# Optimization experiments

Hardware: AMD Instinct MI355X
Metric: run time of the kernel (lower is better)

The kernel has to match this reference:

```python
import jax, jax.numpy as jnp
import numpy as np

D = 4096      # per-region feature dim (input_feature_dims)
OBJ = 20      # regions per frame (memory row = 20*4096)
M = 1000      # temporal_mem_size
K = 1         # temporal_K


def l2norm(x, axis=-1, eps=1e-12):
    # torch F.normalize: x / clamp_min(||x||, eps)
    n = jnp.linalg.norm(x, axis=axis, keepdims=True)
    return x / jnp.maximum(n, eps)


def setup_inputs() -> dict:
    key = jax.random.key(0)
    k1, k2, k3, k4, k5 = jax.random.split(key, 5)
    B, Q, F_ = 4, 4, 20
    return {
        "QR_frm_weight_p": jax.random.normal(k1, (B, Q, F_), jnp.float32),
        "input_pos_feature": jax.random.normal(k2, (B, F_, OBJ, D), jnp.float32),
        "mem1": jax.random.normal(k3, (M, OBJ * D), jnp.float32),
        "mem2": jax.random.normal(k4, (M, OBJ * D), jnp.float32),
        "rand_idx": jax.random.randint(k5, (B, Q, K), 0, F_ - K),
    }


def reference(QR_frm_weight_p, input_pos_feature, mem1, mem2, rand_idx):
    B, Q, F_ = QR_frm_weight_p.shape

    # top-K high-attention frames and a random low-attention frame per query
    _, high_idx = jax.lax.top_k(QR_frm_weight_p, K)              # [B,Q,K]
    _, low_all = jax.lax.top_k(-QR_frm_weight_p, F_ - K)         # smallest, asc
    low_idx = jnp.take_along_axis(low_all, rand_idx, axis=-1)    # [B,Q,K]

    # CVPR feature branch: L2-normalize region features
    R = l2norm(input_pos_feature)                                # [B,F,OBJ,D]

    # max-pool over regions, L2-normalize, then nearest memory slot
    R_max = l2norm(jnp.max(R, axis=2).reshape(-1, D))            # [B*F, D]
    mem1_mp = l2norm(jnp.max(mem1.reshape(M, OBJ, D), axis=1))   # [M, D]
    mem2_mp = l2norm(jnp.max(mem2.reshape(M, OBJ, D), axis=1))   # [M, D]
    sim1 = jnp.argmax(R_max @ mem1_mp.T, axis=-1)                # [B*F]
    Rp_updated = mem1[sim1].reshape(B, F_, OBJ, D)
    sim2 = jnp.argmax(R_max @ mem2_mp.T, axis=-1)
    Rn_updated = mem2[sim2].reshape(B, F_, OBJ, D)

    b_ix = jnp.arange(B)[:, None, None]                          # [B,1,1]
    q_ix = jnp.arange(Q)[None, :, None]                          # [1,Q,1]

    # gather selected frames: [B,Q,K,OBJ,D] -> [Q,B,K,OBJ,D]
    R_high = jnp.transpose(R[b_ix, high_idx], (1, 0, 2, 3, 4))
    R_low = jnp.transpose(R[b_ix, low_idx], (1, 0, 2, 3, 4))

    # Rn: copy of R per query, high-attention frames replaced by mem2
    # counterfactuals gathered at LOW indices (as in the torch code, where
    # `splits` still holds the low-region splits at that point).
    Rn = jnp.broadcast_to(R[:, None], (B, Q, F_, OBJ, D))
    Rn = Rn.at[b_ix, q_ix, high_idx].set(Rn_updated[b_ix, low_idx])
    Rn = jnp.transpose(Rn, (1, 0, 2, 3, 4))                      # [Q,B,F,OBJ,D]

    # Rp: low-attention frames replaced by mem1 entries at low indices
    Rp = jnp.broadcast_to(R[:, None], (B, Q, F_, OBJ, D))
    Rp = Rp.at[b_ix, q_ix, low_idx].set(Rp_updated[b_ix, low_idx])
    Rp = jnp.transpose(Rp, (1, 0, 2, 3, 4))                      # [Q,B,F,OBJ,D]

    # nearest-memory assignment for selected high/low frames
    R_high_mp = l2norm(jnp.max(R_high.reshape(-1, OBJ, D), axis=1))
    R_low_mp = l2norm(jnp.max(R_low.reshape(-1, OBJ, D), axis=1))
    high_sim = jnp.argmax(R_high_mp @ mem2_mp.T, axis=-1)        # [Q*B*K]
    low_sim = jnp.argmax(R_low_mp @ mem1_mp.T, axis=-1)

    return Rp, Rn, high_sim, low_sim
```

## Files before the change

### kernel.cpp

```cpp
#include <hip/hip_runtime.h>

#define D 4096
#define OBJ 20
#define M_MEM 1000
#define F_ 20
#define FRAME_F4 20480
#define RP_F4 6553600
#define OUT_TAIL 52428800

typedef float vf4 __attribute__((ext_vector_type(4)));

__device__ __forceinline__ float4 f4max(float4 a, float4 b){
  return make_float4(fmaxf(a.x,b.x), fmaxf(a.y,b.y), fmaxf(a.z,b.z), fmaxf(a.w,b.w));
}
__device__ __forceinline__ float4 f4scale(float4 a, float s){
  return make_float4(a.x*s, a.y*s, a.z*s, a.w*s);
}
__device__ __forceinline__ double f4ss(float4 a){
  return (double)a.x*a.x + (double)a.y*a.y + (double)a.z*a.z + (double)a.w*a.w;
}
__device__ __forceinline__ void ntst(float4* p, float4 v){
  vf4 t; t.x = v.x; t.y = v.y; t.z = v.z; t.w = v.w;
  __builtin_nontemporal_store(t, (vf4*)p);
}
__device__ __forceinline__ float4 ntld(const float4* p){
  vf4 t = __builtin_nontemporal_load((const vf4*)p);
  return make_float4(t.x, t.y, t.z, t.w);
}

__device__ __forceinline__ unsigned int fkey(float f){
  unsigned int b = __float_as_uint(f);
  return (b & 0x80000000u) ? ~b : (b | 0x80000000u);
}

__device__ __forceinline__ double blockReduce256(double v){
  #pragma unroll
  for (int off = 32; off > 0; off >>= 1) v += __shfl_down(v, off, 64);
  __shared__ double sh[4];
  int w = threadIdx.x >> 6;
  if ((threadIdx.x & 63) == 0) sh[w] = v;
  __syncthreads();
  return sh[0] + sh[1] + sh[2] + sh[3];
}

__global__ void k_fused1(const float* __restrict__ x,
                         const float* __restrict__ mem1, const float* __restrict__ mem2,
                         const float* __restrict__ qr, const int* __restrict__ rand_idx,
                         float* __restrict__ mpn1, float* __restrict__ mpn2,
                         float* __restrict__ rmaxn, float* __restrict__ inv_norm,
                         unsigned long long* __restrict__ packed,
                         int* __restrict__ high_idx, int* __restrict__ low_idx){
  int blk = blockIdx.x;
  int tid = threadIdx.x;
  if (blk >= 80 && blk < 2080){
    int id = blk - 80;
    const float* mem; float* outp; int m;
    if (id < M_MEM){ mem = mem1; outp = mpn1; m = id; }
    else           { mem = mem2; outp = mpn2; m = id - M_MEM; }
    const float4* base = (const float4*)mem + (size_t)m * FRAME_F4;
    float4 mv[4];
    #pragma unroll
    for (int i = 0; i < 4; i++) mv[i] = make_float4(-INFINITY,-INFINITY,-INFINITY,-INFINITY);
    for (int o = 0; o < OBJ; o++){
      const float4* p = base + o*1024;
      #pragma unroll
      for (int i = 0; i < 4; i++) mv[i] = f4max(mv[i], ntld(p + tid + i*256));
    }
    double ss = 0.0;
    #pragma unroll
    for (int i = 0; i < 4; i++) ss += f4ss(mv[i]);
    ss = blockReduce256(ss);
    float rinv = (float)(1.0 / fmax(sqrt(ss), 1e-12));
    float4* o4 = (float4*)outp + (size_t)m * 1024;
    #pragma unroll
    for (int i = 0; i < 4; i++) o4[tid + i*256] = f4scale(mv[i], rinv);
  } else if (blk < 80){
    __shared__ float sinv[OBJ];
    int w = tid >> 6, lane = tid & 63;
    const float4* base = (const float4*)x + (size_t)blk * FRAME_F4;
    for (int o = w*5; o < w*5 + 5; o++){
      const float4* p = base + o*1024;
      double ss = 0.0;
      #pragma unroll
      for (int j = 0; j < 16; j++) ss += f4ss(__ldg(p + j*64 + lane));
      #pragma unroll
      for (int off = 32; off > 0; off >>= 1) ss += __shfl_down(ss, off, 64);
      if (lane == 0){
        float inv = (float)(1.0 / fmax(sqrt(ss), 1e-12));
        sinv[o] = inv;
        inv_norm[blk*OBJ + o] = inv;
      }
    }
    __syncthreads();
    float4 mv[4];
    #pragma unroll
    for (int i = 0; i < 4; i++) mv[i] = make_float4(-INFINITY,-INFINITY,-INFINITY,-INFINITY);
    for (int o = 0; o < OBJ; o++){
      float s = sinv[o];
      const float4* p = base + o*1024;
      #pragma unroll
      for (int i = 0; i < 4; i++) mv[i] = f4max(mv[i], f4scale(__ldg(p + tid + i*256), s));
    }
    double ss = 0.0;
    #pragma unroll
    for (int i = 0; i < 4; i++) ss += f4ss(mv[i]);
    ss = blockReduce256(ss);
    float rinv = (float)(1.0 / fmax(sqrt(ss), 1e-12));
    float4* outp = (float4*)rmaxn + (size_t)blk * 1024;
    #pragma unroll
    for (int i = 0; i < 4; i++) outp[tid + i*256] = f4scale(mv[i], rinv);
  } else {
    int t = tid;
    if (t < 160) packed[t] = 0ull;
    if (t < 16){
      float wv[F_];
      for (int f = 0; f < F_; f++) wv[f] = qr[t*F_ + f];
      int hi = 0; float hv = wv[0];
      for (int f = 1; f < F_; f++) if (wv[f] > hv){ hv = wv[f]; hi = f; }
      int r = rand_idx[t];
      bool used[F_];
      for (int f = 0; f < F_; f++) used[f] = false;
      used[hi] = true;
      int li = 0;
      for (int it = 0; it <= r; it++){
        int bi = -1; float bv = INFINITY;
        for (int f = 0; f < F_; f++) if (!used[f] && wv[f] < bv){ bv = wv[f]; bi = f; }
        used[bi] = true; li = bi;
      }
      high_idx[t] = hi; low_idx[t] = li;
    }
  }
}

__global__ void __launch_bounds__(256, 2)
k_dots(const float* __restrict__ mpn1, const float* __restrict__ mpn2,
       const float* __restrict__ rmaxn,
       unsigned long long* __restrict__ packed){
  int blk = blockIdx.x;
  int which = blk / 250;
  int chunk = blk % 250;
  const float* mpn = which ? mpn2 : mpn1;
  __shared__ float4 rows[4*1024];
  const float4* src = (const float4*)mpn + (size_t)chunk * 4096;
  for (int i = threadIdx.x; i < 4096; i += 256) rows[i] = ntld(src + i);
  __syncthreads();
  int w = threadIdx.x >> 6, lane = threadIdx.x & 63;
  const float4* rbase = (const float4*)rmaxn + (size_t)(w*20) * 1024 + lane;
  float acc[20][4];
  #pragma unroll
  for (int j = 0; j < 20; j++){
    acc[j][0] = 0.f; acc[j][1] = 0.f; acc[j][2] = 0.f; acc[j][3] = 0.f;
  }
  for (int i = 0; i < 16; i++){
    float4 m0 = rows[       i*64 + lane];
    float4 m1 = rows[1024 + i*64 + lane];
    float4 m2 = rows[2048 + i*64 + lane];
    float4 m3 = rows[3072 + i*64 + lane];
    #pragma unroll
    for (int j = 0; j < 20; j++){
      float4 r = __ldg(rbase + (size_t)j*1024 + i*64);
      acc[j][0] += r.x*m0.x + r.y*m0.y + r.z*m0.z + r.w*m0.w;
      acc[j][1] += r.x*m1.x + r.y*m1.y + r.z*m1.z + r.w*m1.w;
      acc[j][2] += r.x*m2.x + r.y*m2.y + r.z*m2.z + r.w*m2.w;
      acc[j][3] += r.x*m3.x + r.y*m3.y + r.z*m3.z + r.w*m3.w;
    }
  }
  unsigned long long* slot = packed + which*80 + w*20;
  #pragma unroll
  for (int j = 0; j < 20; j++){
    float s0 = acc[j][0], s1 = acc[j][1], s2 = acc[j][2], s3 = acc[j][3];
    #pragma unroll
    for (int off = 32; off > 0; off >>= 1){
      s0 += __shfl_down(s0, off, 64);
      s1 += __shfl_down(s1, off, 64);
      s2 += __shfl_down(s2, off, 64);
      s3 += __shfl_down(s3, off, 64);
    }
    if (lane == 0){
      float best = s0; int bi = 0;
      if (s1 > best){ best = s1; bi = 1; }
      if (s2 > best){ best = s2; bi = 2; }
      if (s3 > best){ best = s3; bi = 3; }
      unsigned long long pk = ((unsigned long long)fkey(best) << 32) |
                              (unsigned int)(chunk*4 + bi);
      atomicMax(slot + j, pk);
    }
  }
}

__global__ void k_write(const float* __restrict__ x, const float* __restrict__ inv_norm,
                        const float* __restrict__ mem1, const float* __restrict__ mem2,
                        const int* __restrict__ high_idx, const int* __restrict__ low_idx,
                        const unsigned long long* __restrict__ packed,
                        float* __restrict__ outp){
  int bid = blockIdx.x;
  int tid = threadIdx.x;
  int fid = bid >> 3;
  int part = bid & 7;
  int q = fid / 80;
  int rem = fid - q*80;
  int b = rem / F_;
  int f = rem - b*F_;
  int t16 = b*4 + q;
  int lo = __ldg(low_idx + t16), hi = __ldg(high_idx + t16);

  if (bid == 0 && tid < 16){
    int tb = tid >> 2, tq = tid & 3;
    int thi = __ldg(high_idx + tid), tlo = __ldg(low_idx + tid);
    int s2hi = (int)(unsigned int)__ldg(packed + 80 + tb*F_ + thi);
    int s1lo = (int)(unsigned int)__ldg(packed +      tb*F_ + tlo);
    outp[OUT_TAIL      + tq*4 + tb] = (float)s2hi;
    outp[OUT_TAIL + 16 + tq*4 + tb] = (float)s1lo;
  }

  __shared__ float sinv[OBJ];
  if (tid < OBJ) sinv[tid] = inv_norm[(b*F_ + f)*OBJ + tid];
  __syncthreads();

  const float4* xf = (const float4*)x + (size_t)(b*F_ + f)*FRAME_F4;
  float4* o4 = (float4*)outp;
  size_t fbase = (size_t)fid * FRAME_F4;

  if (f == lo){
    int rpRow = (int)(unsigned int)__ldg(packed + b*F_ + lo);
    const float4* m1p = (const float4*)mem1 + (size_t)rpRow * FRAME_F4;
    #pragma unroll
    for (int k = 0; k < 10; k++){
      int e4 = part*2560 + k*256 + tid;
      float s = sinv[(part*10 + k) >> 2];
      float4 xn = f4scale(__ldg(xf + e4), s);
      ntst(o4 + fbase + e4, __ldg(m1p + e4));
      ntst(o4 + RP_F4 + fbase + e4, xn);
    }
  } else if (f == hi){
    int rnRow = (int)(unsigned int)__ldg(packed + 80 + b*F_ + lo);
    const float4* m2p = (const float4*)mem2 + (size_t)rnRow * FRAME_F4;
    #pragma unroll
    for (int k = 0; k < 10; k++){
      int e4 = part*2560 + k*256 + tid;
      float s = sinv[(part*10 + k) >> 2];
      float4 xn = f4scale(__ldg(xf + e4), s);
      ntst(o4 + fbase + e4, xn);
      ntst(o4 + RP_F4 + fbase + e4, __ldg(m2p + e4));
    }
  } else {
    #pragma unroll
    for (int k = 0; k < 10; k++){
      int e4 = part*2560 + k*256 + tid;
      float s = sinv[(part*10 + k) >> 2];
      float4 xn = f4scale(__ldg(xf + e4), s);
      ntst(o4 + fbase + e4, xn);
      ntst(o4 + RP_F4 + fbase + e4, xn);
    }
  }
}

extern "C" void kernel_launch(void* const* d_in, const int* in_sizes, int n_in,
                              void* d_out, int out_size, void* d_ws, size_t ws_size,
                              hipStream_t stream) {
  const float* qr       = (const float*)d_in[0];
  const float* x        = (const float*)d_in[1];
  const float* mem1     = (const float*)d_in[2];
  const float* mem2     = (const float*)d_in[3];
  const int*   rand_idx = (const int*)  d_in[4];
  float* outp = (float*)d_out;

  float* mpn1     = (float*)d_ws;
  float* mpn2     = mpn1 + 4096000;
  float* rmaxn    = mpn2 + 4096000;
  float* inv_norm = rmaxn + 327680;
  unsigned long long* packed = (unsigned long long*)(inv_norm + 1600);
  int*   high_idx = (int*)(packed + 160);
  int*   low_idx  = high_idx + 16;

  k_fused1<<<2081, 256, 0, stream>>>(x, mem1, mem2, qr, rand_idx,
                                     mpn1, mpn2, rmaxn, inv_norm,
                                     packed, high_idx, low_idx);
  k_dots  <<<500,  256, 0, stream>>>(mpn1, mpn2, rmaxn, packed);
  k_write <<<2560, 256, 0, stream>>>(x, inv_norm, mem1, mem2,
                                     high_idx, low_idx, packed, outp);
}
```

Before: 792.1 us.

## Reuse normalized frame across all queries in write kernel; drop LDS staging in dots

```diff
diff --git a/kernel.cpp b/kernel.cpp
--- a/kernel.cpp
+++ b/kernel.cpp
@@ -132,18 +132,14 @@
   }
 }
 
-__global__ void __launch_bounds__(256, 2)
+__global__ void __launch_bounds__(256, 3)
 k_dots(const float* __restrict__ mpn1, const float* __restrict__ mpn2,
        const float* __restrict__ rmaxn,
        unsigned long long* __restrict__ packed){
   int blk = blockIdx.x;
   int which = blk / 250;
   int chunk = blk % 250;
-  const float* mpn = which ? mpn2 : mpn1;
-  __shared__ float4 rows[4*1024];
-  const float4* src = (const float4*)mpn + (size_t)chunk * 4096;
-  for (int i = threadIdx.x; i < 4096; i += 256) rows[i] = ntld(src + i);
-  __syncthreads();
+  const float4* mrow = (const float4*)(which ? mpn2 : mpn1) + (size_t)chunk * 4096;
   int w = threadIdx.x >> 6, lane = threadIdx.x & 63;
   const float4* rbase = (const float4*)rmaxn + (size_t)(w*20) * 1024 + lane;
   float acc[20][4];
@@ -152,10 +148,10 @@
     acc[j][0] = 0.f; acc[j][1] = 0.f; acc[j][2] = 0.f; acc[j][3] = 0.f;
   }
   for (int i = 0; i < 16; i++){
-    float4 m0 = rows[       i*64 + lane];
-    float4 m1 = rows[1024 + i*64 + lane];
-    float4 m2 = rows[2048 + i*64 + lane];
-    float4 m3 = rows[3072 + i*64 + lane];
+    float4 m0 = __ldg(mrow +        i*64 + lane);
+    float4 m1 = __ldg(mrow + 1024 + i*64 + lane);
+    float4 m2 = __ldg(mrow + 2048 + i*64 + lane);
+    float4 m3 = __ldg(mrow + 3072 + i*64 + lane);
     #pragma unroll
     for (int j = 0; j < 20; j++){
       float4 r = __ldg(rbase + (size_t)j*1024 + i*64);
@@ -195,14 +191,10 @@
                         float* __restrict__ outp){
   int bid = blockIdx.x;
   int tid = threadIdx.x;
-  int fid = bid >> 3;
   int part = bid & 7;
-  int q = fid / 80;
-  int rem = fid - q*80;
-  int b = rem / F_;
-  int f = rem - b*F_;
-  int t16 = b*4 + q;
-  int lo = __ldg(low_idx + t16), hi = __ldg(high_idx + t16);
+  int bf = bid >> 3;
+  int b = bf / F_;
+  int f = bf - b*F_;
 
   if (bid == 0 && tid < 16){
     int tb = tid >> 2, tq = tid & 3;
@@ -214,43 +206,40 @@
   }
 
   __shared__ float sinv[OBJ];
-  if (tid < OBJ) sinv[tid] = inv_norm[(b*F_ + f)*OBJ + tid];
+  if (tid < OBJ) sinv[tid] = inv_norm[bf*OBJ + tid];
   __syncthreads();
 
-  const float4* xf = (const float4*)x + (size_t)(b*F_ + f)*FRAME_F4;
+  const float4* rpS[4];
+  const float4* rnS[4];
+  #pragma unroll
+  for (int q = 0; q < 4; q++){
+    int t16 = b*4 + q;
+    int loq = __ldg(low_idx + t16), hiq = __ldg(high_idx + t16);
+    rpS[q] = nullptr; rnS[q] = nullptr;
+    if (f == loq){
+      int row = (int)(unsigned int)__ldg(packed + b*F_ + loq);
+      rpS[q] = (const float4*)mem1 + (size_t)row * FRAME_F4;
+    }
+    if (f == hiq){
+      int row = (int)(unsigned int)__ldg(packed + 80 + b*F_ + loq);
+      rnS[q] = (const float4*)mem2 + (size_t)row * FRAME_F4;
+    }
+  }
+
+  const float4* xf = (const float4*)x + (size_t)bf * FRAME_F4;
   float4* o4 = (float4*)outp;
-  size_t fbase = (size_t)fid * FRAME_F4;
-
-  if (f == lo){
-    int rpRow = (int)(unsigned int)__ldg(packed + b*F_ + lo);
-    const float4* m1p = (const float4*)mem1 + (size_t)rpRow * FRAME_F4;
-    #pragma unroll
-    for (int k = 0; k < 10; k++){
-      int e4 = part*2560 + k*256 + tid;
-      float s = sinv[(part*10 + k) >> 2];
-      float4 xn = f4scale(__ldg(xf + e4), s);
-      ntst(o4 + fbase + e4, __ldg(m1p + e4));
-      ntst(o4 + RP_F4 + fbase + e4, xn);
-    }
-  } else if (f == hi){
-    int rnRow = (int)(unsigned int)__ldg(packed + 80 + b*F_ + lo);
-    const float4* m2p = (const float4*)mem2 + (size_t)rnRow * FRAME_F4;
-    #pragma unroll
-    for (int k = 0; k < 10; k++){
-      int e4 = part*2560 + k*256 + tid;
-      float s = sinv[(part*10 + k) >> 2];
-      float4 xn = f4scale(__ldg(xf + e4), s);
-      ntst(o4 + fbase + e4, xn);
-      ntst(o4 + RP_F4 + fbase + e4, __ldg(m2p + e4));
-    }
-  } else {
-    #pragma unroll
-    for (int k = 0; k < 10; k++){
-      int e4 = part*2560 + k*256 + tid;
-      float s = sinv[(part*10 + k) >> 2];
-      float4 xn = f4scale(__ldg(xf + e4), s);
-      ntst(o4 + fbase + e4, xn);
-      ntst(o4 + RP_F4 + fbase + e4, xn);
+
+  for (int k = 0; k < 10; k++){
+    int e4 = part*2560 + k*256 + tid;
+    float s = sinv[(part*10 + k) >> 2];
+    float4 xn = f4scale(__ldg(xf + e4), s);
+    #pragma unroll
+    for (int q = 0; q < 4; q++){
+      size_t fb = (size_t)(q*80 + bf) * FRAME_F4;
+      float4 rp = rpS[q] ? __ldg(rpS[q] + e4) : xn;
+      float4 rn = rnS[q] ? __ldg(rnS[q] + e4) : xn;
+      ntst(o4 + fb + e4, rp);
+      ntst(o4 + RP_F4 + fb + e4, rn);
     }
   }
 }
@@ -277,6 +266,6 @@
                                      mpn1, mpn2, rmaxn, inv_norm,
                                      packed, high_idx, low_idx);
   k_dots  <<<500,  256, 0, stream>>>(mpn1, mpn2, rmaxn, packed);
-  k_write <<<2560, 256, 0, stream>>>(x, inv_norm, mem1, mem2,
+  k_write <<<640,  256, 0, stream>>>(x, inv_norm, mem1, mem2,
                                      high_idx, low_idx, packed, outp);
 }
```

After: 879.4 us. 11.0% more time.
